# Kernel optimization log

Measured on AMD Instinct MI355X. Metric: run time of the kernel, lower is better.

The kernel has to match this reference:

```python
import jax, jax.numpy as jnp
import numpy as np

N, D, H, E, K, C = 8192, 1024, 2048, 8, 2, 2560  # tokens, d_model, hidden, experts, top_k, capacity


def setup_inputs() -> dict:
    key = jax.random.key(0)
    ks = jax.random.split(key, 8)
    s_in, s_h = 1.0 / np.sqrt(D), 1.0 / np.sqrt(H)
    return {
        "x": jax.random.normal(ks[0], (N, D), jnp.float32),
        "Wg": jax.random.uniform(ks[1], (D, E), jnp.float32, -s_in, s_in),
        "bg": jnp.zeros((E,), jnp.float32),
        "W1": jax.random.uniform(ks[2], (E, D, H), jnp.float32, -s_in, s_in),
        "b1": jnp.zeros((E, H), jnp.float32),
        "W2": jax.random.uniform(ks[3], (E, H, H), jnp.float32, -s_h, s_h),
        "b2": jnp.zeros((E, H), jnp.float32),
    }


def reference(x, Wg, bg, W1, b1, W2, b2):
    n = x.shape[0]
    logits = x @ Wg + bg                                  # [N, E]
    probs = jax.nn.softmax(logits, axis=-1)
    topk_probs, topk_idx = jax.lax.top_k(probs, K)        # [N, K]

    # auxiliary losses (training mode)
    importance = probs.sum(0)
    importance_loss = jnp.var(importance) / (E ** 2)
    rows = jnp.arange(n)[:, None]
    mask = jnp.zeros_like(probs).at[rows, topk_idx].set(1.0)
    routing_probs = probs * mask
    expert_usage = mask.mean(0)
    routing_weights = routing_probs.mean(0)
    load_balance_loss = E * (expert_usage * routing_weights).sum()
    aux_loss = importance_loss + load_balance_loss

    # dispatch: rank of each (token, k) slot within its expert, in flat order
    flat_e = topk_idx.reshape(-1)                          # [N*K]
    flat_p = topk_probs.reshape(-1)                        # [N*K]
    sample_idx = jnp.repeat(jnp.arange(n), K)              # [N*K]
    oh = (flat_e[:, None] == jnp.arange(E)[None, :]).astype(jnp.int32)  # [N*K, E]
    rank = jnp.take_along_axis(jnp.cumsum(oh, axis=0), flat_e[:, None], axis=1)[:, 0] - 1
    keep = rank < C                                        # capacity truncation (first-come)
    r_safe = jnp.where(keep, rank, C)                      # C is out-of-bounds -> dropped

    buf = jnp.zeros((E, C, D), x.dtype).at[flat_e, r_safe].set(x[sample_idx], mode="drop")
    h = jax.nn.gelu(jnp.einsum("ecd,edh->ech", buf, W1) + b1[:, None, :], approximate=False)
    y = jnp.einsum("ech,eho->eco", h, W2) + b2[:, None, :]  # [E, C, H]

    gathered = y[flat_e, jnp.minimum(r_safe, C - 1)]       # [N*K, H]
    weighted = gathered * (flat_p * keep.astype(x.dtype))[:, None]
    outputs = jnp.zeros((n, H), x.dtype).at[sample_idx].add(weighted)
    return outputs, aux_loss
```

## Files before the change

### kernel.cpp

```cpp
#include <hip/hip_runtime.h>
#include <math.h>
#include <stdint.h>

#define N_TOK 8192
#define DMODEL 1024
#define HID 2048
#define NEXP 8
#define TOPK 2
#define CAP 2560
#define NTILES 640

typedef __bf16 bf16x8 __attribute__((ext_vector_type(8)));
typedef float f32x4 __attribute__((ext_vector_type(4)));
typedef unsigned int u32x4 __attribute__((ext_vector_type(4)));

__device__ __forceinline__ unsigned short f2b(float f) {
    unsigned int u = __builtin_bit_cast(unsigned int, f);
    u += 0x7fffu + ((u >> 16) & 1u);
    return (unsigned short)(u >> 16);
}
__device__ __forceinline__ float b2f(unsigned short s) {
    unsigned int u = ((unsigned int)s) << 16;
    return __builtin_bit_cast(float, u);
}

__device__ __forceinline__ float gelu_f(float v) {
    const float ax = fabsf(v) * 0.70710678118654752440f;
    const float t = __builtin_amdgcn_rcpf(1.f + 0.3275911f * ax);
    float poly = ((((1.061405429f * t - 1.453152027f) * t + 1.421413741f) * t
                   - 0.284496736f) * t + 0.254829592f) * t;
    float er = 1.f - poly * __expf(-ax * ax);
    er = (v >= 0.f) ? er : -er;
    return 0.5f * v * (1.f + er);
}

__device__ __forceinline__ void gload_lds16(const void* g, void* lds) {
    __builtin_amdgcn_global_load_lds(
        (const __attribute__((address_space(1))) unsigned int*)(uintptr_t)g,
        (__attribute__((address_space(3))) unsigned int*)(unsigned int)(uintptr_t)lds,
        16, 0, 0);
}

__global__ __launch_bounds__(256) void gate_kernel(
    const float* __restrict__ x, const float* __restrict__ Wg,
    const float* __restrict__ bg,
    int* __restrict__ flat_e, float* __restrict__ flat_p,
    float* __restrict__ imp_part, float* __restrict__ sel_part,
    unsigned short* __restrict__ xbf)
{
    __shared__ float s_imp[4][NEXP];
    __shared__ float s_sel[4][NEXP];
    const int wave = threadIdx.x >> 6;
    const int lane = threadIdx.x & 63;
    const int t = blockIdx.x * 4 + wave;

    float acc[NEXP];
#pragma unroll
    for (int e = 0; e < NEXP; ++e) acc[e] = 0.f;
    const float* xr = x + (size_t)t * DMODEL;
    unsigned short* xbr = xbf + (size_t)t * DMODEL;
    for (int d = lane; d < DMODEL; d += 64) {
        const float xv = xr[d];
        xbr[d] = f2b(xv);
#pragma unroll
        for (int e = 0; e < NEXP; ++e) acc[e] += xv * Wg[d * NEXP + e];
    }
#pragma unroll
    for (int off = 32; off > 0; off >>= 1) {
#pragma unroll
        for (int e = 0; e < NEXP; ++e) acc[e] += __shfl_xor(acc[e], off);
    }
    float lg[NEXP], mx = -1e30f;
#pragma unroll
    for (int e = 0; e < NEXP; ++e) { lg[e] = acc[e] + bg[e]; mx = fmaxf(mx, lg[e]); }
    float p[NEXP], s = 0.f;
#pragma unroll
    for (int e = 0; e < NEXP; ++e) { p[e] = expf(lg[e] - mx); s += p[e]; }
    const float inv = 1.f / s;
#pragma unroll
    for (int e = 0; e < NEXP; ++e) p[e] *= inv;

    int i0 = 0;
#pragma unroll
    for (int e = 1; e < NEXP; ++e) if (p[e] > p[i0]) i0 = e;
    int i1 = (i0 == 0) ? 1 : 0;
#pragma unroll
    for (int e = 0; e < NEXP; ++e) if (e != i0 && p[e] > p[i1]) i1 = e;

    if (lane == 0) {
        flat_e[2 * t] = i0;  flat_e[2 * t + 1] = i1;
        flat_p[2 * t] = p[i0]; flat_p[2 * t + 1] = p[i1];
#pragma unroll
        for (int e = 0; e < NEXP; ++e) {
            s_imp[wave][e] = p[e];
            s_sel[wave][e] = (e == i0) ? p[i0] : ((e == i1) ? p[i1] : 0.f);
        }
    }
    __syncthreads();
    if (threadIdx.x < NEXP) {
        const int e = threadIdx.x;
        float a = 0.f, b = 0.f;
#pragma unroll
        for (int w = 0; w < 4; ++w) { a += s_imp[w][e]; b += s_sel[w][e]; }
        imp_part[blockIdx.x * NEXP + e] = a;
        sel_part[blockIdx.x * NEXP + e] = b;
    }
}

__global__ __launch_bounds__(1024) void scan_kernel(
    const int* __restrict__ flat_e, int* __restrict__ slot_rank,
    int* __restrict__ row_token, int* __restrict__ n_kept,
    int* __restrict__ cnt_full, unsigned short* __restrict__ xbf_pad,
    int* __restrict__ ctrs)
{
    __shared__ int wave_tot[16][NEXP];
    __shared__ int base[NEXP];
    const int tid = threadIdx.x, lane = tid & 63, w = tid >> 6;
    if (tid < NEXP) base[tid] = 0;
    if (tid < 2) ctrs[tid] = 0;
    for (int i = tid; i < DMODEL; i += 1024) xbf_pad[i] = 0;
    __syncthreads();
    const unsigned long long ltmask =
        (lane == 0) ? 0ull : (~0ull >> (64 - lane));
    for (int chunk = 0; chunk < (N_TOK * TOPK) / 1024; ++chunk) {
        const int s = chunk * 1024 + tid;
        const int e = flat_e[s];
        int prefix = 0;
#pragma unroll
        for (int ee = 0; ee < NEXP; ++ee) {
            unsigned long long m = __ballot(e == ee);
            if (ee == e) prefix = __popcll(m & ltmask);
            if (lane == 0) wave_tot[w][ee] = __popcll(m);
        }
        __syncthreads();
        int before = base[e];
        for (int ww = 0; ww < w; ++ww) before += wave_tot[ww][e];
        const int rank = before + prefix;
        slot_rank[s] = rank;
        if (rank < CAP) row_token[e * CAP + rank] = s >> 1;
        __syncthreads();
        if (tid < NEXP) {
            int add = 0;
#pragma unroll
            for (int ww = 0; ww < 16; ++ww) add += wave_tot[ww][tid];
            base[tid] += add;
        }
        __syncthreads();
    }
    for (int i = tid; i < NEXP * CAP; i += 1024) {
        const int ee = i / CAP;
        const int r = i - ee * CAP;
        const int ne = base[ee] < CAP ? base[ee] : CAP;
        if (r >= ne) row_token[i] = N_TOK;
    }
    if (tid < NEXP) {
        n_kept[tid] = min(base[tid], CAP);
        cnt_full[tid] = base[tid];
    }
}

__global__ __launch_bounds__(256) void transpose_cvt(
    const float* __restrict__ W, unsigned short* __restrict__ Wt,
    const int R, const int Cdim)
{
    __shared__ unsigned short s[64][66];
    const int e = blockIdx.z;
    const int c0 = blockIdx.x * 64, r0 = blockIdx.y * 64;
    const float* We = W + (size_t)e * R * Cdim;
    unsigned short* Wte = Wt + (size_t)e * R * Cdim;
    const int tid = threadIdx.x;
    const int lr = tid >> 6;
    const int lc = tid & 63;
#pragma unroll
    for (int i = 0; i < 16; ++i)
        s[lr + i * 4][lc] =
            f2b(__builtin_nontemporal_load(&We[(size_t)(r0 + lr + i * 4) * Cdim + c0 + lc]));
    __syncthreads();
#pragma unroll
    for (int pass = 0; pass < 2; ++pass) {
        const int cc = (tid >> 3) + pass * 32;
        const int rq = (tid & 7) * 8;
        unsigned short v[8];
#pragma unroll
        for (int k = 0; k < 8; ++k) v[k] = s[rq + k][cc];
        u32x4 o;
        o[0] = v[0] | ((unsigned)v[1] << 16); o[1] = v[2] | ((unsigned)v[3] << 16);
        o[2] = v[4] | ((unsigned)v[5] << 16); o[3] = v[6] | ((unsigned)v[7] << 16);
        *(u32x4*)&Wte[(size_t)(c0 + cc) * R + r0 + rq] = o;
    }
}

#define VMGATE4() do { asm volatile("s_waitcnt vmcnt(4)" ::: "memory"); \
                       __builtin_amdgcn_sched_barrier(0); } while (0)
#define VMGATE0() do { asm volatile("s_waitcnt vmcnt(0)" ::: "memory"); \
                       __builtin_amdgcn_sched_barrier(0); } while (0)
#define NOGATE() ((void)0)

#define PHASE(mf0, STAGE_STMT, TAIL_STMT) do {                                   \
    bf16x8 a0 = lda(c, (mf0), 0), a1 = lda(c, (mf0), 1);                         \
    bf16x8 a2 = lda(c, (mf0) + 1, 0), a3 = lda(c, (mf0) + 1, 1);                 \
    STAGE_STMT;                                                                  \
    __builtin_amdgcn_s_barrier();                                                \
    asm volatile("s_waitcnt lgkmcnt(0)" ::: "memory");                           \
    __builtin_amdgcn_sched_barrier(0);                                           \
    __builtin_amdgcn_s_setprio(1);                                               \
    _Pragma("unroll")                                                            \
    for (int nf = 0; nf < 4; ++nf) {                                             \
        acc[(mf0)][nf] = __builtin_amdgcn_mfma_f32_16x16x32_bf16(                \
            a0, bfr[nf][0], acc[(mf0)][nf], 0, 0, 0);                            \
        acc[(mf0)][nf] = __builtin_amdgcn_mfma_f32_16x16x32_bf16(                \
            a1, bfr[nf][1], acc[(mf0)][nf], 0, 0, 0);                            \
        acc[(mf0) + 1][nf] = __builtin_amdgcn_mfma_f32_16x16x32_bf16(            \
            a2, bfr[nf][0], acc[(mf0) + 1][nf], 0, 0, 0);                        \
        acc[(mf0) + 1][nf] = __builtin_amdgcn_mfma_f32_16x16x32_bf16(            \
            a3, bfr[nf][1], acc[(mf0) + 1][nf], 0, 0, 0);                        \
    }                                                                            \
    __builtin_amdgcn_s_setprio(0);                                               \
    TAIL_STMT;                                                                   \
    __builtin_amdgcn_s_barrier();                                                \
} while (0)

template <bool GATHER, bool DO_GELU>
__global__ __launch_bounds__(512, 1) void mfma_gemm256(
    const unsigned short* __restrict__ A,
    const unsigned short* __restrict__ Wt,
    const float* __restrict__ bias,
    unsigned short* __restrict__ out,
    const int* __restrict__ row_token, const int* __restrict__ n_kept,
    int* __restrict__ ctr, const int Kdim)
{
    __shared__ unsigned short smem[81920];
    int* s_item = (int*)((char*)smem + 163836);

    const int t = threadIdx.x;
    const int w = t >> 6, lane = t & 63;
    const int wm = w >> 2, wn = w & 3;
    const int l15 = lane & 15, lq = lane >> 4;
    const int srow_lo = t >> 3;
    const int NT = Kdim >> 6;

    const int sx = (l15 & 4) << 3;
    const int kbx0 = (lq * 16) ^ sx;
    const int kbx1 = (64 + lq * 16) ^ sx;
    auto lda = [&](int cbuf, int mf, int ks) -> bf16x8 {
        return *(const bf16x8*)((const char*)smem + cbuf * 32768 +
                                (wm * 128 + mf * 16 + l15) * 128 + (ks ? kbx1 : kbx0));
    };
    auto ldb = [&](int cbuf, int nf, int ks) -> bf16x8 {
        return *(const bf16x8*)((const char*)smem + 65536 + cbuf * 32768 +
                                (wn * 64 + nf * 16 + l15) * 128 + (ks ? kbx1 : kbx0));
    };

    for (;;) {
        __syncthreads();
        if (t == 0) *s_item = atomicAdd(ctr, 1);
        __syncthreads();
        const int item = *s_item;
        if (item >= NTILES) break;

        const int e = item / 80;
        const int rem = item - e * 80;
        const int m = rem % 10;
        const int n = rem / 10;
        const int m0 = m * 256, n0 = n * 256;
        const int n_e = n_kept[e];
        if (m0 >= n_e) continue;

        long abase[2][2], bbase[2][2];
#pragma unroll
        for (int h = 0; h < 2; ++h) {
#pragma unroll
            for (int cc = 0; cc < 2; ++cc) {
                const int srow = h * 128 + cc * 64 + srow_lo;
                const int skoff = ((t & 7) * 8) ^ ((srow & 4) << 2);
                long ar;
                if (GATHER) ar = (long)row_token[e * CAP + m0 + srow] * Kdim;
                else        ar = ((long)e * CAP + m0 + srow) * (long)Kdim;
                abase[h][cc] = ar + skoff;
                bbase[h][cc] = ((long)e * HID + n0 + srow) * (long)Kdim + skoff;
            }
        }
        auto stageA = [&](int buf, int h0, int ktile) {
            const long ko = (long)ktile * 64;
            char* base = (char*)smem + buf * 32768 + h0 * 16384 + w * 1024;
            gload_lds16(A + (h0 ? abase[1][0] : abase[0][0]) + ko, base);
            gload_lds16(A + (h0 ? abase[1][1] : abase[0][1]) + ko, base + 8192);
        };
        auto stageB = [&](int buf, int h0, int ktile) {
            const long ko = (long)ktile * 64;
            char* base = (char*)smem + 65536 + buf * 32768 + h0 * 16384 + w * 1024;
            gload_lds16(Wt + (h0 ? bbase[1][0] : bbase[0][0]) + ko, base);
            gload_lds16(Wt + (h0 ? bbase[1][1] : bbase[0][1]) + ko, base + 8192);
        };

        f32x4 acc[8][4];
#pragma unroll
        for (int mm = 0; mm < 8; ++mm)
#pragma unroll
            for (int nn = 0; nn < 4; ++nn) acc[mm][nn] = (f32x4)0.f;

        stageA(0, 0, 0); stageA(0, 1, 0);
        stageB(0, 0, 0); stageB(0, 1, 0);
        stageB(1, 0, 1); stageB(1, 1, 1);
        VMGATE4();
        __builtin_amdgcn_s_barrier();

        int bcur = 0;
        for (int kt = 0; kt < NT; ++kt) {
            const int c = kt & 1, o = c ^ 1;
            const int ktA = kt + 1;
            const int ktB = kt + 2;
            int bst = bcur + 2; if (bst >= 3) bst -= 3;

            bf16x8 bfr[4][2];
#pragma unroll
            for (int nf = 0; nf < 4; ++nf) {
                bfr[nf][0] = ldb(bcur, nf, 0);
                bfr[nf][1] = ldb(bcur, nf, 1);
            }
            PHASE(0, if (ktA < NT) stageA(o, 0, ktA), NOGATE());
            PHASE(2, if (ktA < NT) stageA(o, 1, ktA), NOGATE());
            PHASE(4, if (ktB < NT) stageB(bst, 0, ktB), NOGATE());
            if (ktB < NT) {
                PHASE(6, stageB(bst, 1, ktB), VMGATE4());
            } else {
                PHASE(6, NOGATE(), VMGATE0());
            }
            bcur = (bcur == 2) ? 0 : bcur + 1;
        }

        const float* be = bias + (size_t)e * HID;
        float bv[4];
#pragma unroll
        for (int nf = 0; nf < 4; ++nf)
            bv[nf] = be[n0 + wn * 64 + nf * 16 + l15];
#pragma unroll
        for (int mf = 0; mf < 8; ++mf) {
#pragma unroll
            for (int j = 0; j < 4; ++j) {
                const int row = m0 + wm * 128 + mf * 16 + lq * 4 + j;
                unsigned short* orow =
                    out + ((size_t)e * CAP + row) * HID + n0 + wn * 64 + l15;
#pragma unroll
                for (int nf = 0; nf < 4; ++nf) {
                    float v = acc[mf][nf][j] + bv[nf];
                    if (DO_GELU) v = gelu_f(v);
                    orow[nf * 16] = f2b(v);
                }
            }
        }
    }
}

__global__ __launch_bounds__(256) void combine_kernel(
    const unsigned short* __restrict__ y, const int* __restrict__ flat_e,
    const float* __restrict__ flat_p, const int* __restrict__ slot_rank,
    float* __restrict__ out)
{
    const int t = blockIdx.x;
    const int e0 = flat_e[2 * t], e1 = flat_e[2 * t + 1];
    const int r0 = slot_rank[2 * t], r1 = slot_rank[2 * t + 1];
    const bool k0 = r0 < CAP, k1 = r1 < CAP;
    const float w0 = k0 ? flat_p[2 * t] : 0.f;
    const float w1 = k1 ? flat_p[2 * t + 1] : 0.f;
    const unsigned short* y0 = y + ((size_t)e0 * CAP + (k0 ? r0 : 0)) * HID;
    const unsigned short* y1 = y + ((size_t)e1 * CAP + (k1 ? r1 : 0)) * HID;
    float* orow = out + (size_t)t * HID;
    const int c = threadIdx.x * 8;
    u32x4 av = k0 ? __builtin_nontemporal_load((const u32x4*)(y0 + c)) : (u32x4)0u;
    u32x4 bv = k1 ? __builtin_nontemporal_load((const u32x4*)(y1 + c)) : (u32x4)0u;
    float o[8];
    auto comb2 = [&](unsigned int a, unsigned int b, float* dst) {
        dst[0] = w0 * b2f((unsigned short)(a & 0xffffu)) +
                 w1 * b2f((unsigned short)(b & 0xffffu));
        dst[1] = w0 * b2f((unsigned short)(a >> 16)) +
                 w1 * b2f((unsigned short)(b >> 16));
    };
    comb2(av[0], bv[0], o + 0); comb2(av[1], bv[1], o + 2);
    comb2(av[2], bv[2], o + 4); comb2(av[3], bv[3], o + 6);
    f32x4 o0 = {o[0], o[1], o[2], o[3]};
    f32x4 o1 = {o[4], o[5], o[6], o[7]};
    __builtin_nontemporal_store(o0, (f32x4*)(orow + c));
    __builtin_nontemporal_store(o1, (f32x4*)(orow + c + 4));
}

__global__ __launch_bounds__(64) void aux_kernel(
    const float* __restrict__ imp_part, const float* __restrict__ sel_part,
    const int* __restrict__ cnt_full, float* __restrict__ out_aux,
    const int nparts)
{
    const int lane = threadIdx.x;
    __shared__ float imp_s[NEXP], sel_s[NEXP];
    for (int e = 0; e < NEXP; ++e) {
        float a = 0.f, b = 0.f;
        for (int i = lane; i < nparts; i += 64) {
            a += imp_part[i * NEXP + e];
            b += sel_part[i * NEXP + e];
        }
#pragma unroll
        for (int off = 32; off > 0; off >>= 1) {
            a += __shfl_xor(a, off);
            b += __shfl_xor(b, off);
        }
        if (lane == 0) { imp_s[e] = a; sel_s[e] = b; }
    }
    __syncthreads();
    if (lane == 0) {
        double mean = 0.0;
        for (int e = 0; e < NEXP; ++e) mean += imp_s[e];
        mean /= NEXP;
        double var = 0.0;
        for (int e = 0; e < NEXP; ++e) {
            const double d = (double)imp_s[e] - mean;
            var += d * d;
        }
        var /= NEXP;
        double load = 0.0;
        for (int e = 0; e < NEXP; ++e)
            load += ((double)cnt_full[e] / N_TOK) * ((double)sel_s[e] / N_TOK);
        load *= NEXP;
        out_aux[0] = (float)(var / (NEXP * NEXP) + load);
    }
}

extern "C" void kernel_launch(void* const* d_in, const int* in_sizes, int n_in,
                              void* d_out, int out_size, void* d_ws, size_t ws_size,
                              hipStream_t stream) {
    const float* x  = (const float*)d_in[0];
    const float* Wg = (const float*)d_in[1];
    const float* bg = (const float*)d_in[2];
    const float* W1 = (const float*)d_in[3];
    const float* b1 = (const float*)d_in[4];
    const float* W2 = (const float*)d_in[5];
    const float* b2 = (const float*)d_in[6];
    float* out = (float*)d_out;
    (void)in_sizes; (void)n_in; (void)out_size; (void)ws_size;

    char* ws = (char*)d_ws;
    size_t off = 0;
    auto alloc = [&](size_t bytes) -> void* {
        void* p = ws + off;
        off = (off + bytes + 255) & ~(size_t)255;
        return p;
    };
    int*   n_kept    = (int*)alloc(NEXP * sizeof(int));
    int*   cnt_full  = (int*)alloc(NEXP * sizeof(int));
    int*   ctrs     = (int*)alloc(2 * sizeof(int));
    int*   flat_e    = (int*)alloc((size_t)N_TOK * TOPK * sizeof(int));
    float* flat_p    = (float*)alloc((size_t)N_TOK * TOPK * sizeof(float));
    int*   slot_rank = (int*)alloc((size_t)N_TOK * TOPK * sizeof(int));
    int*   row_tok   = (int*)alloc((size_t)NEXP * CAP * sizeof(int));
    float* imp_part  = (float*)alloc((size_t)(N_TOK / 4) * NEXP * sizeof(float));
    float* sel_part  = (float*)alloc((size_t)(N_TOK / 4) * NEXP * sizeof(float));
    unsigned short* xbf  = (unsigned short*)alloc((size_t)(N_TOK + 1) * DMODEL * 2);
    unsigned short* w1t  = (unsigned short*)alloc((size_t)NEXP * DMODEL * HID * 2);
    unsigned short* w2t  = (unsigned short*)alloc((size_t)NEXP * HID * HID * 2);
    unsigned short* hbuf = (unsigned short*)alloc((size_t)NEXP * CAP * HID * 2);
    unsigned short* ybuf = (unsigned short*)alloc((size_t)NEXP * CAP * HID * 2);

    gate_kernel<<<N_TOK / 4, 256, 0, stream>>>(x, Wg, bg, flat_e, flat_p,
                                               imp_part, sel_part, xbf);
    scan_kernel<<<1, 1024, 0, stream>>>(flat_e, slot_rank, row_tok, n_kept,
                                        cnt_full, xbf + (size_t)N_TOK * DMODEL,
                                        ctrs);

    transpose_cvt<<<dim3(HID / 64, DMODEL / 64, NEXP), 256, 0, stream>>>(W1, w1t, DMODEL, HID);
    mfma_gemm256<true,  true ><<<256, 512, 0, stream>>>(
        xbf,  w1t, b1, hbuf, row_tok, n_kept, ctrs + 0, DMODEL);

    transpose_cvt<<<dim3(HID / 64, HID / 64, NEXP), 256, 0, stream>>>(W2, w2t, HID, HID);
    mfma_gemm256<false, false><<<256, 512, 0, stream>>>(
        hbuf, w2t, b2, ybuf, row_tok, n_kept, ctrs + 1, HID);

    combine_kernel<<<N_TOK, 256, 0, stream>>>(ybuf, flat_e, flat_p, slot_rank, out);
    aux_kernel<<<1, 64, 0, stream>>>(imp_part, sel_part, cnt_full,
                                     out + (size_t)N_TOK * HID, N_TOK / 4);
}
```

Baseline: 479.2 us.

## Fuse combine into second expert GEMM epilogue with weighted atomic adds

Removes the separate combine kernel and the bf16 y buffer. The scan kernel now records a per-row routing weight, the gate kernel zero-fills the output, and the second GEMM's epilogue atomically adds the weighted result into each token's output row. This drops a full write and read of the E×C×H intermediate, and y is no longer rounded to bf16 before combining. In exchange it issues scalar fp32 atomics with strided per-row scatter, and the summation order becomes nondeterministic.

```diff
diff --git a/kernel.cpp b/kernel.cpp
--- a/kernel.cpp
+++ b/kernel.cpp
@@ -46,7 +46,7 @@
     const float* __restrict__ bg,
     int* __restrict__ flat_e, float* __restrict__ flat_p,
     float* __restrict__ imp_part, float* __restrict__ sel_part,
-    unsigned short* __restrict__ xbf)
+    unsigned short* __restrict__ xbf, float* __restrict__ out)
 {
     __shared__ float s_imp[4][NEXP];
     __shared__ float s_sel[4][NEXP];
@@ -54,6 +54,11 @@
     const int lane = threadIdx.x & 63;
     const int t = blockIdx.x * 4 + wave;
 
+    float* orow = out + (size_t)t * HID;
+#pragma unroll
+    for (int i = 0; i < 8; ++i)
+        *(f32x4*)(orow + i * 256 + lane * 4) = (f32x4)0.f;
+
     float acc[NEXP];
 #pragma unroll
     for (int e = 0; e < NEXP; ++e) acc[e] = 0.f;
@@ -108,10 +113,10 @@
 }
 
 __global__ __launch_bounds__(1024) void scan_kernel(
-    const int* __restrict__ flat_e, int* __restrict__ slot_rank,
-    int* __restrict__ row_token, int* __restrict__ n_kept,
-    int* __restrict__ cnt_full, unsigned short* __restrict__ xbf_pad,
-    int* __restrict__ ctrs)
+    const int* __restrict__ flat_e, const float* __restrict__ flat_p,
+    int* __restrict__ row_token, float* __restrict__ wrow,
+    int* __restrict__ n_kept, int* __restrict__ cnt_full,
+    unsigned short* __restrict__ xbf_pad, int* __restrict__ ctrs)
 {
     __shared__ int wave_tot[16][NEXP];
     __shared__ int base[NEXP];
@@ -136,8 +141,10 @@
         int before = base[e];
         for (int ww = 0; ww < w; ++ww) before += wave_tot[ww][e];
         const int rank = before + prefix;
-        slot_rank[s] = rank;
-        if (rank < CAP) row_token[e * CAP + rank] = s >> 1;
+        if (rank < CAP) {
+            row_token[e * CAP + rank] = s >> 1;
+            wrow[e * CAP + rank] = flat_p[s];
+        }
         __syncthreads();
         if (tid < NEXP) {
             int add = 0;
@@ -151,7 +158,7 @@
         const int ee = i / CAP;
         const int r = i - ee * CAP;
         const int ne = base[ee] < CAP ? base[ee] : CAP;
-        if (r >= ne) row_token[i] = N_TOK;
+        if (r >= ne) { row_token[i] = N_TOK; wrow[i] = 0.f; }
     }
     if (tid < NEXP) {
         n_kept[tid] = min(base[tid], CAP);
@@ -220,13 +227,15 @@
     __builtin_amdgcn_s_barrier();                                                \
 } while (0)
 
-template <bool GATHER, bool DO_GELU>
+template <bool GATHER, bool DO_GELU, bool COMBINE>
 __global__ __launch_bounds__(512, 1) void mfma_gemm256(
     const unsigned short* __restrict__ A,
     const unsigned short* __restrict__ Wt,
     const float* __restrict__ bias,
-    unsigned short* __restrict__ out,
-    const int* __restrict__ row_token, const int* __restrict__ n_kept,
+    unsigned short* __restrict__ outb,
+    float* __restrict__ outf,
+    const int* __restrict__ row_token, const float* __restrict__ wrow,
+    const int* __restrict__ n_kept,
     int* __restrict__ ctr, const int Kdim)
 {
     __shared__ unsigned short smem[81920];
@@ -339,49 +348,30 @@
 #pragma unroll
             for (int j = 0; j < 4; ++j) {
                 const int row = m0 + wm * 128 + mf * 16 + lq * 4 + j;
-                unsigned short* orow =
-                    out + ((size_t)e * CAP + row) * HID + n0 + wn * 64 + l15;
-#pragma unroll
-                for (int nf = 0; nf < 4; ++nf) {
-                    float v = acc[mf][nf][j] + bv[nf];
-                    if (DO_GELU) v = gelu_f(v);
-                    orow[nf * 16] = f2b(v);
+                if (COMBINE) {
+                    const int tok = row_token[e * CAP + row];
+                    const float wgt = wrow[e * CAP + row];
+                    if (wgt != 0.f) {
+                        float* orow = outf + (size_t)tok * HID + n0 + wn * 64 + l15;
+#pragma unroll
+                        for (int nf = 0; nf < 4; ++nf) {
+                            const float v = acc[mf][nf][j] + bv[nf];
+                            atomicAdd(&orow[nf * 16], wgt * v);
+                        }
+                    }
+                } else {
+                    unsigned short* orow =
+                        outb + ((size_t)e * CAP + row) * HID + n0 + wn * 64 + l15;
+#pragma unroll
+                    for (int nf = 0; nf < 4; ++nf) {
+                        float v = acc[mf][nf][j] + bv[nf];
+                        if (DO_GELU) v = gelu_f(v);
+                        orow[nf * 16] = f2b(v);
+                    }
                 }
             }
         }
     }
-}
-
-__global__ __launch_bounds__(256) void combine_kernel(
-    const unsigned short* __restrict__ y, const int* __restrict__ flat_e,
-    const float* __restrict__ flat_p, const int* __restrict__ slot_rank,
-    float* __restrict__ out)
-{
-    const int t = blockIdx.x;
-    const int e0 = flat_e[2 * t], e1 = flat_e[2 * t + 1];
-    const int r0 = slot_rank[2 * t], r1 = slot_rank[2 * t + 1];
-    const bool k0 = r0 < CAP, k1 = r1 < CAP;
-    const float w0 = k0 ? flat_p[2 * t] : 0.f;
-    const float w1 = k1 ? flat_p[2 * t + 1] : 0.f;
-    const unsigned short* y0 = y + ((size_t)e0 * CAP + (k0 ? r0 : 0)) * HID;
-    const unsigned short* y1 = y + ((size_t)e1 * CAP + (k1 ? r1 : 0)) * HID;
-    float* orow = out + (size_t)t * HID;
-    const int c = threadIdx.x * 8;
-    u32x4 av = k0 ? __builtin_nontemporal_load((const u32x4*)(y0 + c)) : (u32x4)0u;
-    u32x4 bv = k1 ? __builtin_nontemporal_load((const u32x4*)(y1 + c)) : (u32x4)0u;
-    float o[8];
-    auto comb2 = [&](unsigned int a, unsigned int b, float* dst) {
-        dst[0] = w0 * b2f((unsigned short)(a & 0xffffu)) +
-                 w1 * b2f((unsigned short)(b & 0xffffu));
-        dst[1] = w0 * b2f((unsigned short)(a >> 16)) +
-                 w1 * b2f((unsigned short)(b >> 16));
-    };
-    comb2(av[0], bv[0], o + 0); comb2(av[1], bv[1], o + 2);
-    comb2(av[2], bv[2], o + 4); comb2(av[3], bv[3], o + 6);
-    f32x4 o0 = {o[0], o[1], o[2], o[3]};
-    f32x4 o1 = {o[4], o[5], o[6], o[7]};
-    __builtin_nontemporal_store(o0, (f32x4*)(orow + c));
-    __builtin_nontemporal_store(o1, (f32x4*)(orow + c + 4));
 }
 
 __global__ __launch_bounds__(64) void aux_kernel(
@@ -445,34 +435,32 @@
     };
     int*   n_kept    = (int*)alloc(NEXP * sizeof(int));
     int*   cnt_full  = (int*)alloc(NEXP * sizeof(int));
-    int*   ctrs     = (int*)alloc(2 * sizeof(int));
+    int*   ctrs      = (int*)alloc(2 * sizeof(int));
     int*   flat_e    = (int*)alloc((size_t)N_TOK * TOPK * sizeof(int));
     float* flat_p    = (float*)alloc((size_t)N_TOK * TOPK * sizeof(float));
-    int*   slot_rank = (int*)alloc((size_t)N_TOK * TOPK * sizeof(int));
     int*   row_tok   = (int*)alloc((size_t)NEXP * CAP * sizeof(int));
+    float* wrow      = (float*)alloc((size_t)NEXP * CAP * sizeof(float));
     float* imp_part  = (float*)alloc((size_t)(N_TOK / 4) * NEXP * sizeof(float));
     float* sel_part  = (float*)alloc((size_t)(N_TOK / 4) * NEXP * sizeof(float));
     unsigned short* xbf  = (unsigned short*)alloc((size_t)(N_TOK + 1) * DMODEL * 2);
     unsigned short* w1t  = (unsigned short*)alloc((size_t)NEXP * DMODEL * HID * 2);
     unsigned short* w2t  = (unsigned short*)alloc((size_t)NEXP * HID * HID * 2);
     unsigned short* hbuf = (unsigned short*)alloc((size_t)NEXP * CAP * HID * 2);
-    unsigned short* ybuf = (unsigned short*)alloc((size_t)NEXP * CAP * HID * 2);
 
     gate_kernel<<<N_TOK / 4, 256, 0, stream>>>(x, Wg, bg, flat_e, flat_p,
-                                               imp_part, sel_part, xbf);
-    scan_kernel<<<1, 1024, 0, stream>>>(flat_e, slot_rank, row_tok, n_kept,
+                                               imp_part, sel_part, xbf, out);
+    scan_kernel<<<1, 1024, 0, stream>>>(flat_e, flat_p, row_tok, wrow, n_kept,
                                         cnt_full, xbf + (size_t)N_TOK * DMODEL,
                                         ctrs);
 
     transpose_cvt<<<dim3(HID / 64, DMODEL / 64, NEXP), 256, 0, stream>>>(W1, w1t, DMODEL, HID);
-    mfma_gemm256<true,  true ><<<256, 512, 0, stream>>>(
-        xbf,  w1t, b1, hbuf, row_tok, n_kept, ctrs + 0, DMODEL);
+    mfma_gemm256<true,  true,  false><<<256, 512, 0, stream>>>(
+        xbf,  w1t, b1, hbuf, nullptr, row_tok, wrow, n_kept, ctrs + 0, DMODEL);
 
     transpose_cvt<<<dim3(HID / 64, HID / 64, NEXP), 256, 0, stream>>>(W2, w2t, HID, HID);
-    mfma_gemm256<false, false><<<256, 512, 0, stream>>>(
-        hbuf, w2t, b2, ybuf, row_tok, n_kept, ctrs + 1, HID);
-
-    combine_kernel<<<N_TOK, 256, 0, stream>>>(ybuf, flat_e, flat_p, slot_rank, out);
+    mfma_gemm256<false, false, true ><<<256, 512, 0, stream>>>(
+        hbuf, w2t, b2, nullptr, out, row_tok, wrow, n_kept, ctrs + 1, HID);
+
     aux_kernel<<<1, 64, 0, stream>>>(imp_part, sel_part, cnt_full,
                                      out + (size_t)N_TOK * HID, N_TOK / 4);
 }
```

Result: slower. 573.6 us (+19.7%).

## Fuse both expert GEMMs into one persistent kernel with per-row-block dependency flags

Applied to the files above, without the earlier changes.

Merges the two expert GEMM launches into one persistent kernel. It pulls GEMM1 tiles first and then GEMM2 tiles from a shared atomic work counter. Each GEMM2 tile spins on a per-(expert, row-block) counter until all 8 GEMM1 column tiles for those rows have published with release semantics. This removes the kernel boundary and tail bubble between the two GEMMs and lets GEMM2 tiles start while GEMM1 is still finishing. The cost is spin-waiting, runtime branching on Kdim and pointers inside the hot kernel, and a dependence on the GEMM1-first ordering to avoid deadlock.

```diff
diff --git a/kernel.cpp b/kernel.cpp
--- a/kernel.cpp
+++ b/kernel.cpp
@@ -8,7 +8,8 @@
 #define NEXP 8
 #define TOPK 2
 #define CAP 2560
-#define NTILES 640
+#define NT1 640
+#define NTALL 1280
 
 typedef __bf16 bf16x8 __attribute__((ext_vector_type(8)));
 typedef float f32x4 __attribute__((ext_vector_type(4)));
@@ -117,7 +118,7 @@
     __shared__ int base[NEXP];
     const int tid = threadIdx.x, lane = tid & 63, w = tid >> 6;
     if (tid < NEXP) base[tid] = 0;
-    if (tid < 2) ctrs[tid] = 0;
+    if (tid < 81) ctrs[tid] = 0;
     for (int i = tid; i < DMODEL; i += 1024) xbf_pad[i] = 0;
     __syncthreads();
     const unsigned long long ltmask =
@@ -220,24 +221,25 @@
     __builtin_amdgcn_s_barrier();                                                \
 } while (0)
 
-template <bool GATHER, bool DO_GELU>
-__global__ __launch_bounds__(512, 1) void mfma_gemm256(
-    const unsigned short* __restrict__ A,
-    const unsigned short* __restrict__ Wt,
-    const float* __restrict__ bias,
-    unsigned short* __restrict__ out,
+__global__ __launch_bounds__(512, 1) void mfma_gemm_fused(
+    const unsigned short* __restrict__ xbf,
+    const unsigned short* __restrict__ w1t,
+    const unsigned short* __restrict__ w2t,
+    const float* __restrict__ b1, const float* __restrict__ b2,
+    unsigned short* __restrict__ hbuf,
+    unsigned short* __restrict__ ybuf,
     const int* __restrict__ row_token, const int* __restrict__ n_kept,
-    int* __restrict__ ctr, const int Kdim)
+    int* __restrict__ ctr)
 {
     __shared__ unsigned short smem[81920];
     int* s_item = (int*)((char*)smem + 163836);
+    int* done = ctr + 1;
 
     const int t = threadIdx.x;
     const int w = t >> 6, lane = t & 63;
     const int wm = w >> 2, wn = w & 3;
     const int l15 = lane & 15, lq = lane >> 4;
     const int srow_lo = t >> 3;
-    const int NT = Kdim >> 6;
 
     const int sx = (l15 & 4) << 3;
     const int kbx0 = (lq * 16) ^ sx;
@@ -256,15 +258,30 @@
         if (t == 0) *s_item = atomicAdd(ctr, 1);
         __syncthreads();
         const int item = *s_item;
-        if (item >= NTILES) break;
-
-        const int e = item / 80;
-        const int rem = item - e * 80;
+        if (item >= NTALL) break;
+
+        const bool g2 = item >= NT1;
+        const int it = g2 ? item - NT1 : item;
+        const int e = it / 80;
+        const int rem = it - e * 80;
         const int m = rem % 10;
         const int n = rem / 10;
         const int m0 = m * 256, n0 = n * 256;
-        const int n_e = n_kept[e];
-        if (m0 >= n_e) continue;
+        if (m0 >= n_kept[e]) continue;
+
+        if (g2) {
+            if (t == 0) {
+                while (__hip_atomic_load(&done[e * 10 + m], __ATOMIC_ACQUIRE,
+                                         __HIP_MEMORY_SCOPE_AGENT) < 8)
+                    __builtin_amdgcn_s_sleep(8);
+            }
+            __syncthreads();
+        }
+
+        const int Kdim = g2 ? HID : DMODEL;
+        const int NT = Kdim >> 6;
+        const unsigned short* A  = g2 ? hbuf : xbf;
+        const unsigned short* Wt = g2 ? w2t : w1t;
 
         long abase[2][2], bbase[2][2];
 #pragma unroll
@@ -274,8 +291,8 @@
                 const int srow = h * 128 + cc * 64 + srow_lo;
                 const int skoff = ((t & 7) * 8) ^ ((srow & 4) << 2);
                 long ar;
-                if (GATHER) ar = (long)row_token[e * CAP + m0 + srow] * Kdim;
-                else        ar = ((long)e * CAP + m0 + srow) * (long)Kdim;
+                if (g2) ar = ((long)e * CAP + m0 + srow) * (long)Kdim;
+                else    ar = (long)row_token[e * CAP + m0 + srow] * Kdim;
                 abase[h][cc] = ar + skoff;
                 bbase[h][cc] = ((long)e * HID + n0 + srow) * (long)Kdim + skoff;
             }
@@ -329,7 +346,8 @@
             bcur = (bcur == 2) ? 0 : bcur + 1;
         }
 
-        const float* be = bias + (size_t)e * HID;
+        const float* be = (g2 ? b2 : b1) + (size_t)e * HID;
+        unsigned short* outp = g2 ? ybuf : hbuf;
         float bv[4];
 #pragma unroll
         for (int nf = 0; nf < 4; ++nf)
@@ -340,14 +358,21 @@
             for (int j = 0; j < 4; ++j) {
                 const int row = m0 + wm * 128 + mf * 16 + lq * 4 + j;
                 unsigned short* orow =
-                    out + ((size_t)e * CAP + row) * HID + n0 + wn * 64 + l15;
+                    outp + ((size_t)e * CAP + row) * HID + n0 + wn * 64 + l15;
 #pragma unroll
                 for (int nf = 0; nf < 4; ++nf) {
                     float v = acc[mf][nf][j] + bv[nf];
-                    if (DO_GELU) v = gelu_f(v);
+                    if (!g2) v = gelu_f(v);
                     orow[nf * 16] = f2b(v);
                 }
             }
+        }
+
+        if (!g2) {
+            __syncthreads();
+            if (t == 0)
+                __hip_atomic_fetch_add(&done[e * 10 + m], 1, __ATOMIC_RELEASE,
+                                       __HIP_MEMORY_SCOPE_AGENT);
         }
     }
 }
@@ -445,7 +470,7 @@
     };
     int*   n_kept    = (int*)alloc(NEXP * sizeof(int));
     int*   cnt_full  = (int*)alloc(NEXP * sizeof(int));
-    int*   ctrs     = (int*)alloc(2 * sizeof(int));
+    int*   ctrs      = (int*)alloc(81 * sizeof(int));
     int*   flat_e    = (int*)alloc((size_t)N_TOK * TOPK * sizeof(int));
     float* flat_p    = (float*)alloc((size_t)N_TOK * TOPK * sizeof(float));
     int*   slot_rank = (int*)alloc((size_t)N_TOK * TOPK * sizeof(int));
@@ -465,12 +490,10 @@
                                         ctrs);
 
     transpose_cvt<<<dim3(HID / 64, DMODEL / 64, NEXP), 256, 0, stream>>>(W1, w1t, DMODEL, HID);
-    mfma_gemm256<true,  true ><<<256, 512, 0, stream>>>(
-        xbf,  w1t, b1, hbuf, row_tok, n_kept, ctrs + 0, DMODEL);
-
     transpose_cvt<<<dim3(HID / 64, HID / 64, NEXP), 256, 0, stream>>>(W2, w2t, HID, HID);
-    mfma_gemm256<false, false><<<256, 512, 0, stream>>>(
-        hbuf, w2t, b2, ybuf, row_tok, n_kept, ctrs + 1, HID);
+
+    mfma_gemm_fused<<<256, 512, 0, stream>>>(xbf, w1t, w2t, b1, b2, hbuf, ybuf,
+                                             row_tok, n_kept, ctrs);
 
     combine_kernel<<<N_TOK, 256, 0, stream>>>(ybuf, flat_e, flat_p, slot_rank, out);
     aux_kernel<<<1, 64, 0, stream>>>(imp_part, sel_part, cnt_full,
```

Measured after the change: 449.2 us (median of 2 runs). 6.3% less time.
